# Kernel optimization log

Hardware: AMD Instinct MI355X
Metric: run time of the kernel (lower is better)

## Reference

```python
import jax, jax.numpy as jnp
import numpy as np

T, N, F, L, A = 4, 16, 6, 1024, 21  # genomes, tiles, frames, tile length, alphabet
K, U = 20, 256                      # profile width, number of profiles


def setup_inputs() -> dict:
    key = jax.random.key(0)
    k1, k2 = jax.random.split(key)
    X = jax.random.uniform(k1, (T, N, F, L, A), dtype=jnp.float32)
    Q = jnp.ones((A,), dtype=jnp.float32) / A  # uniform background distribution
    # P_logit ~ log(Q) + N(0, 4) as in _getRandomProfiles
    P_logit = (jnp.log(Q)[None, :, None]
               + 4.0 * jax.random.normal(k2, (K, A, U), dtype=jnp.float32))
    return {"X": X, "P_logit": P_logit, "Q": Q}


def reference(X, P_logit, Q):
    # SpecificProfile.call(X) -> (S, R, Z)
    Tb, Nb, Fb, Lb, Ab = X.shape
    k, _, units = P_logit.shape
    # getR: P = softmax(P_logit, axis=1); R = log(max(P / Q, epsilon))
    P = jax.nn.softmax(P_logit, axis=1)                    # [k, A, U]
    epsilon = jnp.mean(Q)                                   # exp(-log(1/mean(Q)))
    R = jnp.log(jnp.maximum(P / Q[None, :, None], epsilon))  # [k, A, U]
    # getZ: conv2d over (length, alphabet) spatial dims, VALID padding
    Xr = X.reshape(Tb * Nb * Fb, Lb, Ab, 1)                 # NHWC
    Kr = R[:, :, None, :]                                   # HWIO: [k, A, 1, U]
    Z = jax.lax.conv_general_dilated(
        Xr, Kr, window_strides=(1, 1), padding='VALID',
        dimension_numbers=('NHWC', 'HWIO', 'NHWC'))          # [TNF, L-k+1, 1, U]
    Z = Z.reshape(Tb, Nb, Fb, Lb - k + 1, units)            # [T, N, F, P, U]
    S = jnp.max(Z, axis=(2, 3))                             # [T, N, U]
    return S, R, Z
```

## Files before the change

### kernel.cpp

```cpp
#include <hip/hip_runtime.h>
#include <hip/hip_bf16.h>
#include <math.h>

#define T_ 4
#define N_ 16
#define F_ 6
#define L_ 1024
#define A_ 21
#define K_ 20
#define U_ 256
#define LOUT 1005
#define NIMG 384
#define SZ_S (T_*N_*U_)
#define SZ_R (K_*A_*U_)

#define XPR 24
#define XROWS 1056
#define NSTEP 15
#define XWCH 7

typedef __attribute__((ext_vector_type(8))) short short8;
typedef __attribute__((ext_vector_type(4))) float f32x4;

__device__ __forceinline__ unsigned short f2bf(float f) {
  unsigned int u = __float_as_uint(f);
  u += 0x7FFFu + ((u >> 16) & 1u);
  return (unsigned short)(u >> 16);
}

__device__ __forceinline__ void atomicMaxF(float* addr, float val) {
  if (val >= 0.f) atomicMax((int*)addr, __float_as_int(val));
  else            atomicMin((unsigned int*)addr, __float_as_uint(val));
}

__device__ __forceinline__ void gload_lds16(const void* g, void* l) {
  __builtin_amdgcn_global_load_lds(
      (const __attribute__((address_space(1))) void*)g,
      (__attribute__((address_space(3))) void*)l, 16, 0, 0);
}

__global__ void xprep_kernel(const float* __restrict__ X,
                             const float* __restrict__ P_logit,
                             const float* __restrict__ Q,
                             float* __restrict__ out,
                             unsigned short* __restrict__ Rt,
                             unsigned int* __restrict__ Xp32) {
  int t = blockIdx.x * blockDim.x + threadIdx.x;
  if (t < SZ_S) out[t] = -INFINITY;

  if (t < K_ * U_) {
    int k = t / U_;
    int u = t - k * U_;
    const float* pl = P_logit + (size_t)k * A_ * U_ + u;
    float v[A_];
    float m = -INFINITY;
#pragma unroll
    for (int a = 0; a < A_; ++a) { v[a] = pl[(size_t)a * U_]; m = fmaxf(m, v[a]); }
    float s = 0.f;
#pragma unroll
    for (int a = 0; a < A_; ++a) { v[a] = expf(v[a] - m); s += v[a]; }
    float qs = 0.f;
#pragma unroll
    for (int a = 0; a < A_; ++a) qs += Q[a];
    float eps = qs * (1.0f / A_);
    float invs = 1.f / s;
    float* Rout = out + SZ_S;
#pragma unroll
    for (int a = 0; a < XPR; ++a) {
      unsigned short bv = 0;
      if (a < A_) {
        float r = logf(fmaxf(v[a] * invs / Q[a], eps));
        Rout[(size_t)(k * A_ + a) * U_ + u] = r;
        bv = f2bf(r);
      }
      int sl = k * XPR + a;
      Rt[(size_t)(sl >> 5) * (U_ * 32) + u * 32 + (sl & 31)] = bv;
    }
  }

  if (t < NIMG * XROWS * 12) {
    int w  = t % 12;
    int rl = t / 12;
    int row = rl % XROWS;
    int n   = rl / XROWS;
    int c0 = w * 2;
    float v0 = 0.f, v1 = 0.f;
    if (row < L_) {
      const float* xr = X + ((size_t)n * L_ + row) * A_;
      if (c0 < A_)     v0 = xr[c0];
      if (c0 + 1 < A_) v1 = xr[c0 + 1];
    }
    unsigned int o = (unsigned int)f2bf(v0) | ((unsigned int)f2bf(v1) << 16);
    Xp32[(size_t)rl * 12 + w] = o;
  }
}

__global__ __launch_bounds__(256, 1) void conv_kernel(
    const unsigned short* __restrict__ Xp,
    const unsigned short* __restrict__ Rt,
    float* __restrict__ out) {
  __shared__ __align__(16) unsigned short lds_r[NSTEP * 4096];
  __shared__ __align__(16) unsigned short lds_xp[4][XWCH * 512];

  const int n  = blockIdx.z;
  const int u0 = blockIdx.x * 128;
  const int wid  = threadIdx.x >> 6;
  const int lane = threadIdx.x & 63;
  const int wl = wid >> 1;
  const int wu = wid & 1;

  const char* xsrc = (const char*)Xp +
      ((size_t)n * XROWS + wl * 128) * (XPR * 2);
  const char* rsrc = (const char*)Rt + (size_t)u0 * 64;
  char* xdst = (char*)&lds_xp[wid][0];

#define XSTAGE(T)                                                            \
  {                                                                          \
    const char* xs = xsrc + (size_t)(T) * (256 * XPR * 2);                   \
    _Pragma("unroll")                                                        \
    for (int c = 0; c < XWCH; ++c)                                           \
      gload_lds16(xs + c * 1024 + lane * 16, xdst + c * 1024);               \
  }

  for (int c = wid; c < NSTEP * 8; c += 4)
    gload_lds16(rsrc + (size_t)(c >> 3) * (U_ * 64) + (c & 7) * 1024 + lane * 16,
                (char*)lds_r + c * 1024);
  XSTAGE(0)
  asm volatile("s_waitcnt vmcnt(0)" ::: "memory");
  __builtin_amdgcn_s_barrier();

  const int fl = lane & 15;
  const int fj = lane >> 4;
  const int rfo = (wu * 64 + fl) * 32 + (fj << 3);
  const unsigned short* xb =
      (const unsigned short*)xdst + fl * XPR + (fj << 3);
  const int ug = fj << 2;

  float* Z = out + SZ_S + SZ_R;
  float pmax[4][4];
#pragma unroll
  for (int ut = 0; ut < 4; ++ut)
#pragma unroll
    for (int r = 0; r < 4; ++r) pmax[ut][r] = -INFINITY;

#pragma unroll 1
  for (int t = 0; t < 4; ++t) {
    if (t > 0) asm volatile("s_waitcnt vmcnt(32)" ::: "memory");

    f32x4 acc[4][8];
#pragma unroll
    for (int ut = 0; ut < 4; ++ut)
#pragma unroll
      for (int lt = 0; lt < 8; ++lt)
        acc[ut][lt] = (f32x4){0.f, 0.f, 0.f, 0.f};

#pragma unroll
    for (int k = 0; k < NSTEP; ++k) {
      short8 xfr[8], rfr[4];
      const unsigned short* rb = lds_r + k * 4096 + rfo;
#pragma unroll
      for (int lt = 0; lt < 8; ++lt)
        xfr[lt] = *(const short8*)(xb + lt * (16 * XPR) + k * 32);
#pragma unroll
      for (int ut = 0; ut < 4; ++ut)
        rfr[ut] = *(const short8*)(rb + ut * (16 * 32));
#pragma unroll
      for (int ut = 0; ut < 4; ++ut)
#pragma unroll
        for (int lt = 0; lt < 8; ++lt)
          acc[ut][lt] = __builtin_amdgcn_mfma_f32_16x16x32_bf16(
              rfr[ut], xfr[lt], acc[ut][lt], 0, 0, 0);
    }

    if (t < 3) XSTAGE(t + 1)

#pragma unroll
    for (int lt = 0; lt < 8; ++lt) {
      const int l = t * 256 + wl * 128 + lt * 16 + fl;
      if (l < LOUT) {
        float* zrow = Z + ((size_t)n * LOUT + l) * U_ + u0 + wu * 64 + ug;
#pragma unroll
        for (int ut = 0; ut < 4; ++ut) {
          f32x4 v = acc[ut][lt];
          *(f32x4*)(zrow + ut * 16) = v;
#pragma unroll
          for (int r = 0; r < 4; ++r) pmax[ut][r] = fmaxf(pmax[ut][r], v[r]);
        }
      }
    }
  }

#undef XSTAGE

#pragma unroll
  for (int off = 1; off < 16; off <<= 1)
#pragma unroll
    for (int ut = 0; ut < 4; ++ut)
#pragma unroll
      for (int r = 0; r < 4; ++r)
        pmax[ut][r] = fmaxf(pmax[ut][r], __shfl_xor(pmax[ut][r], off));

  if (fl == 0) {
    const int tn = n / F_;
    float* Sp = out + (size_t)tn * U_ + u0 + wu * 64 + ug;
#pragma unroll
    for (int ut = 0; ut < 4; ++ut)
#pragma unroll
      for (int r = 0; r < 4; ++r)
        atomicMaxF(Sp + ut * 16 + r, pmax[ut][r]);
  }
}

extern "C" void kernel_launch(void* const* d_in, const int* in_sizes, int n_in,
                              void* d_out, int out_size, void* d_ws, size_t ws_size,
                              hipStream_t stream) {
  const float* X       = (const float*)d_in[0];
  const float* P_logit = (const float*)d_in[1];
  const float* Q       = (const float*)d_in[2];
  float* out = (float*)d_out;

  unsigned short* Rt = (unsigned short*)d_ws;
  unsigned short* Xp = (unsigned short*)((char*)d_ws + 262144);

  int xthreads = NIMG * XROWS * 12;
  hipLaunchKernelGGL(xprep_kernel, dim3((xthreads + 255) / 256), dim3(256),
                     0, stream, X, P_logit, Q, out, Rt, (unsigned int*)Xp);
  dim3 grid(2, 1, NIMG);
  hipLaunchKernelGGL(conv_kernel, grid, dim3(256), 0, stream, Xp, Rt, out);
}
```

Before: 140.6 us.

## Double-buffer accumulators to overlap Z stores with next tile's MFMAs

Unrolls the four L-tiles and alternates between two accumulator sets. The Z stores and running max of the previous tile are interleaved with the MFMA k-steps of the current tile. X tiles are now prefetched into registers with ordinary global loads and written to LDS after compute, replacing the async global-to-LDS loads. The goal is to hide the large Z write traffic behind tensor-core work. The cost is doubled accumulator register pressure, which risks spills or heavier AGPR use.

New measurement: 130.9 us. -6.9%, faster.

```diff
diff --git a/kernel.cpp b/kernel.cpp
--- a/kernel.cpp
+++ b/kernel.cpp
@@ -21,6 +21,7 @@
 
 typedef __attribute__((ext_vector_type(8))) short short8;
 typedef __attribute__((ext_vector_type(4))) float f32x4;
+typedef __attribute__((ext_vector_type(4))) unsigned int uint4v;
 
 __device__ __forceinline__ unsigned short f2bf(float f) {
   unsigned int u = __float_as_uint(f);
@@ -114,18 +115,12 @@
   const char* rsrc = (const char*)Rt + (size_t)u0 * 64;
   char* xdst = (char*)&lds_xp[wid][0];
 
-#define XSTAGE(T)                                                            \
-  {                                                                          \
-    const char* xs = xsrc + (size_t)(T) * (256 * XPR * 2);                   \
-    _Pragma("unroll")                                                        \
-    for (int c = 0; c < XWCH; ++c)                                           \
-      gload_lds16(xs + c * 1024 + lane * 16, xdst + c * 1024);               \
-  }
-
   for (int c = wid; c < NSTEP * 8; c += 4)
     gload_lds16(rsrc + (size_t)(c >> 3) * (U_ * 64) + (c & 7) * 1024 + lane * 16,
                 (char*)lds_r + c * 1024);
-  XSTAGE(0)
+#pragma unroll
+  for (int c = 0; c < XWCH; ++c)
+    gload_lds16(xsrc + c * 1024 + lane * 16, xdst + c * 1024);
   asm volatile("s_waitcnt vmcnt(0)" ::: "memory");
   __builtin_amdgcn_s_barrier();
 
@@ -143,54 +138,118 @@
 #pragma unroll
     for (int r = 0; r < 4; ++r) pmax[ut][r] = -INFINITY;
 
-#pragma unroll 1
-  for (int t = 0; t < 4; ++t) {
-    if (t > 0) asm volatile("s_waitcnt vmcnt(32)" ::: "memory");
-
-    f32x4 acc[4][8];
-#pragma unroll
-    for (int ut = 0; ut < 4; ++ut)
-#pragma unroll
-      for (int lt = 0; lt < 8; ++lt)
-        acc[ut][lt] = (f32x4){0.f, 0.f, 0.f, 0.f};
-
-#pragma unroll
-    for (int k = 0; k < NSTEP; ++k) {
-      short8 xfr[8], rfr[4];
-      const unsigned short* rb = lds_r + k * 4096 + rfo;
-#pragma unroll
-      for (int lt = 0; lt < 8; ++lt)
-        xfr[lt] = *(const short8*)(xb + lt * (16 * XPR) + k * 32);
-#pragma unroll
-      for (int ut = 0; ut < 4; ++ut)
-        rfr[ut] = *(const short8*)(rb + ut * (16 * 32));
-#pragma unroll
-      for (int ut = 0; ut < 4; ++ut)
-#pragma unroll
-        for (int lt = 0; lt < 8; ++lt)
-          acc[ut][lt] = __builtin_amdgcn_mfma_f32_16x16x32_bf16(
-              rfr[ut], xfr[lt], acc[ut][lt], 0, 0, 0);
-    }
-
-    if (t < 3) XSTAGE(t + 1)
-
-#pragma unroll
-    for (int lt = 0; lt < 8; ++lt) {
-      const int l = t * 256 + wl * 128 + lt * 16 + fl;
-      if (l < LOUT) {
-        float* zrow = Z + ((size_t)n * LOUT + l) * U_ + u0 + wu * 64 + ug;
-#pragma unroll
-        for (int ut = 0; ut < 4; ++ut) {
-          f32x4 v = acc[ut][lt];
-          *(f32x4*)(zrow + ut * 16) = v;
-#pragma unroll
-          for (int r = 0; r < 4; ++r) pmax[ut][r] = fmaxf(pmax[ut][r], v[r]);
-        }
+  f32x4 accA[4][8], accB[4][8];
+  uint4v xr[XWCH];
+
+#define ZERO(ACC)                                                            \
+  {                                                                          \
+    _Pragma("unroll")                                                        \
+    for (int ut = 0; ut < 4; ++ut)                                           \
+      _Pragma("unroll")                                                      \
+      for (int lt = 0; lt < 8; ++lt)                                         \
+        (ACC)[ut][lt] = (f32x4){0.f, 0.f, 0.f, 0.f};                         \
+  }
+
+#define KSTEP(K, ACC)                                                        \
+  {                                                                          \
+    short8 xfr[8], rfr[4];                                                   \
+    const unsigned short* rb = lds_r + (K) * 4096 + rfo;                     \
+    _Pragma("unroll")                                                        \
+    for (int lt = 0; lt < 8; ++lt)                                           \
+      xfr[lt] = *(const short8*)(xb + lt * (16 * XPR) + (K) * 32);           \
+    _Pragma("unroll")                                                        \
+    for (int ut = 0; ut < 4; ++ut)                                           \
+      rfr[ut] = *(const short8*)(rb + ut * (16 * 32));                       \
+    _Pragma("unroll")                                                        \
+    for (int ut = 0; ut < 4; ++ut)                                           \
+      _Pragma("unroll")                                                      \
+      for (int lt = 0; lt < 8; ++lt)                                         \
+        (ACC)[ut][lt] = __builtin_amdgcn_mfma_f32_16x16x32_bf16(             \
+            rfr[ut], xfr[lt], (ACC)[ut][lt], 0, 0, 0);                       \
+  }
+
+#define STORE4(ACC, TT, LT)                                                  \
+  {                                                                          \
+    const int l = (TT) * 256 + wl * 128 + (LT) * 16 + fl;                    \
+    float* zrow = Z + ((size_t)n * LOUT + l) * U_ + u0 + wu * 64 + ug;       \
+    _Pragma("unroll")                                                        \
+    for (int ut = 0; ut < 4; ++ut) {                                         \
+      f32x4 v = (ACC)[ut][LT];                                               \
+      *(f32x4*)(zrow + ut * 16) = v;                                         \
+      _Pragma("unroll")                                                      \
+      for (int r = 0; r < 4; ++r) pmax[ut][r] = fmaxf(pmax[ut][r], v[r]);    \
+    }                                                                        \
+  }
+
+#define XLOADS(T1)                                                           \
+  {                                                                          \
+    const char* xs = xsrc + (size_t)(T1) * (256 * XPR * 2);                  \
+    _Pragma("unroll")                                                        \
+    for (int c = 0; c < XWCH; ++c)                                           \
+      xr[c] = *(const uint4v*)(xs + c * 1024 + lane * 16);                   \
+  }
+
+#define XWRITE()                                                             \
+  {                                                                          \
+    _Pragma("unroll")                                                        \
+    for (int c = 0; c < XWCH; ++c)                                           \
+      *(uint4v*)(xdst + c * 1024 + lane * 16) = xr[c];                       \
+  }
+
+  ZERO(accA)
+  XLOADS(1)
+#pragma unroll
+  for (int k = 0; k < NSTEP; ++k) KSTEP(k, accA)
+  asm volatile("s_waitcnt vmcnt(0)" ::: "memory");
+  XWRITE()
+
+  ZERO(accB)
+  XLOADS(2)
+#pragma unroll
+  for (int k = 0; k < NSTEP; ++k) {
+    KSTEP(k, accB)
+    if (k >= 1 && k <= 8) STORE4(accA, 0, k - 1)
+  }
+  asm volatile("s_waitcnt vmcnt(32)" ::: "memory");
+  XWRITE()
+
+  ZERO(accA)
+  XLOADS(3)
+#pragma unroll
+  for (int k = 0; k < NSTEP; ++k) {
+    KSTEP(k, accA)
+    if (k >= 1 && k <= 8) STORE4(accB, 1, k - 1)
+  }
+  asm volatile("s_waitcnt vmcnt(32)" ::: "memory");
+  XWRITE()
+
+  ZERO(accB)
+#pragma unroll
+  for (int k = 0; k < NSTEP; ++k) {
+    KSTEP(k, accB)
+    if (k >= 1 && k <= 8) STORE4(accA, 2, k - 1)
+  }
+
+#pragma unroll
+  for (int lt = 0; lt < 8; ++lt) {
+    const int l = 768 + wl * 128 + lt * 16 + fl;
+    if (l < LOUT) {
+      float* zrow = Z + ((size_t)n * LOUT + l) * U_ + u0 + wu * 64 + ug;
+#pragma unroll
+      for (int ut = 0; ut < 4; ++ut) {
+        f32x4 v = accB[ut][lt];
+        *(f32x4*)(zrow + ut * 16) = v;
+#pragma unroll
+        for (int r = 0; r < 4; ++r) pmax[ut][r] = fmaxf(pmax[ut][r], v[r]);
       }
     }
   }
 
-#undef XSTAGE
+#undef ZERO
+#undef KSTEP
+#undef STORE4
+#undef XLOADS
+#undef XWRITE
 
 #pragma unroll
   for (int off = 1; off < 16; off <<= 1)
```
